# Performance work log

Hardware: AMD Instinct MI355X
Metric: run time of the kernel (lower is better)

Reference implementation:

```python
import jax, jax.numpy as jnp
import numpy as np

N_IN = 512
N_OUT = 256
K = 3
GRID_SIZE = N_OUT - K + 1  # 254
X_LO, X_HI = -1.0, 1.0
BATCH = 1024
LN_EPS = 1e-5


def make_grid():
    # grid_values: (n_in, grid_size + 2k + 1), identical rows as in the torch module
    step = (X_HI - X_LO) / GRID_SIZE
    g = jnp.linspace(X_LO - step * K, X_HI + step * K, GRID_SIZE + 2 * K + 1, dtype=jnp.float32)
    return jnp.broadcast_to(g, (N_IN, g.shape[0]))


def setup_inputs() -> dict:
    key = jax.random.key(0)
    k1, k2, k3 = jax.random.split(key, 3)
    x = jax.random.normal(k1, (BATCH, N_IN), dtype=jnp.float32)
    # kaiming-uniform-like scale for the linear weights
    weights = jax.random.normal(k2, (N_OUT, N_IN), dtype=jnp.float32) * (1.0 / np.sqrt(N_IN))
    spline_weights = jax.random.normal(k3, (N_OUT, N_IN, GRID_SIZE + K), dtype=jnp.float32) * (
        1.0 / np.sqrt(N_IN * (GRID_SIZE + K))
    )
    prelu_a = jnp.full((1,), 0.25, dtype=jnp.float32)  # PReLU default init
    return {"x": x, "weights": weights, "spline_weights": spline_weights, "prelu_a": prelu_a}


def reference(x, weights, spline_weights, prelu_a):
    g = make_grid()  # (n_in, P) with P = GRID_SIZE + 2K + 1
    # base branch: tanh(x) @ W^T
    b_out = jnp.tanh(x) @ weights.T  # (B, n_out)

    # Cox-de Boor recursion for B-spline bases
    xe = x[:, :, None]  # (B, n_in, 1)
    bases = ((xe >= g[:, :-1]) & (xe < g[:, 1:])).astype(x.dtype)  # (B, n_in, P-1)
    for k in range(1, K + 1):
        left = g[:, : -(k + 1)]
        right = g[:, k:-1]
        delta = jnp.where(right == left, jnp.ones_like(right), right - left)
        bases = (xe - left) / delta * bases[:, :, :-1] + (
            (g[:, k + 1 :] - xe) / (g[:, k + 1 :] - g[:, 1:-k])
        ) * bases[:, :, 1:]
    # bases: (B, n_in, GRID_SIZE + K)

    # flattened linear == einsum over (n_in, grid) axes
    spline_out = jnp.einsum("big,oig->bo", bases, spline_weights)  # (B, n_out)

    y = b_out + spline_out
    # LayerNorm without affine params
    mu = jnp.mean(y, axis=-1, keepdims=True)
    var = jnp.var(y, axis=-1, keepdims=True)
    yn = (y - mu) / jnp.sqrt(var + LN_EPS)
    # PReLU (single shared slope)
    return jnp.where(yn >= 0, yn, prelu_a[0] * yn)
```

## Files before the change

### kernel.cpp

```cpp
#include <hip/hip_runtime.h>
#include <hip/hip_fp16.h>
#include <math.h>

#define N_IN   512
#define N_OUT  256
#define NCOEF  257
#define BATCH  1024
#define LN_EPS 1e-5f
#define G0F (-1.0f - 3.0f * (2.0f / 254.0f))

#define ROWQ 20
#define NQ   129
#define SLABW (NQ * ROWQ)

#define SLOT(q_, oo_) ((q_) * ROWQ + (((((oo_) >> 2) ^ ((q_) & 3))) << 2) + ((oo_) & 3))

static __device__ __forceinline__ unsigned pk_bf16x2(float a, float b) {
    unsigned ua = ((__float_as_uint(a) + 0x8000u) >> 16) & 0xffffu;
    unsigned ub = (__float_as_uint(b) + 0x8000u) & 0xffff0000u;
    return ua | ub;
}

static __device__ __forceinline__ float dot2bf(unsigned w, unsigned s, float c) {
    float d;
    asm("v_dot2_f32_bf16 %0, %1, %2, %3" : "=v"(d) : "v"(w), "v"(s), "v"(c));
    return d;
}

static __device__ __forceinline__ uint4 spline_pack(float xv) {
    const float e2 = __expf(2.f * xv);
    const float tx = 1.f - 2.f / (e2 + 1.f);
    const float u  = (xv - G0F) * 127.f;
    const bool has = (u >= 0.f) && (u < 260.f);
    const float uf = has ? u : 0.f;
    int m = (int)uf;
    if (m > 259) m = 259;
    const float tt = uf - (float)m;
    const float t2 = tt * tt, t3 = t2 * tt;
    const float omt = 1.f - tt;
    float a0 = omt * omt * omt * (1.f / 6.f);
    float a1 = (3.f * t3 - 6.f * t2 + 4.f) * (1.f / 6.f);
    float a2 = (-3.f * t3 + 3.f * t2 + 3.f * tt + 1.f) * (1.f / 6.f);
    float a3 = t3 * (1.f / 6.f);
    if (!has) { a0 = a1 = a2 = a3 = 0.f; }
    const int pb  = m - 3;
    const int pbc = pb < 0 ? 0 : (pb > 253 ? 253 : pb);
    const int d   = pbc - pb;
    if (d >= 1)  { a0 = a1; a1 = a2; a2 = a3; a3 = 0.f; }
    if (d >= 2)  { a0 = a1; a1 = a2; a2 = a3; a3 = 0.f; }
    if (d >= 3)  { a0 = a1; a1 = a2; a2 = a3; a3 = 0.f; }
    if (d <= -1) { a3 = a2; a2 = a1; a1 = a0; a0 = 0.f; }
    if (d <= -2) { a3 = a2; a2 = a1; a1 = a0; a0 = 0.f; }
    if (d <= -3) { a3 = a2; a2 = a1; a1 = a0; a0 = 0.f; }
    uint4 r;
    if (pbc & 1) {
        r.x = pk_bf16x2(0.f, a0);
        r.y = pk_bf16x2(a1, a2);
        r.z = pk_bf16x2(a3, 0.f);
    } else {
        r.x = pk_bf16x2(a0, a1);
        r.y = pk_bf16x2(a2, a3);
        r.z = 0u;
    }
    r.w = (unsigned)(pbc & ~1) |
          ((unsigned)__half_as_ushort(__float2half(tx)) << 16);
    return r;
}

__global__ __launch_bounds__(1024, 4) void kan_main(
    const float* __restrict__ x, const float* __restrict__ W,
    const float* __restrict__ sw, float* __restrict__ part)
{
    const int bid = blockIdx.x;
    const int oc = bid & 15;
    const int ig = bid >> 4;
    const int o0 = oc * 16, i0 = ig * 32;
    const int t = threadIdx.x;

    __shared__ __align__(16) unsigned slab[2][2][SLABW];
    __shared__ __align__(16) uint4 wpk[2][1024];
    __shared__ float Wl[2][2][16];

    const int wv = t >> 6, l = t & 63;
    const int bl = (l >> 2) & 15, og = l & 3;
    const int soo = t & 15;
    const int sgc = t >> 4;
    const int wsub = t >> 4;

    const float* swrow = sw + ((size_t)(o0 + soo) * N_IN + i0) * NCOEF;
    const float* xp    = x + (size_t)t * N_IN + i0;
    const float* wgp   = W + (size_t)(o0 + (t & 15)) * N_IN + i0 + wsub;

    float4 pf0, pf1;
    float sT0 = 0.f, sT1 = 0.f, Wc = 0.f;
    float2 xn;

#define GLOAD(p) do {                                             \
        const float* _r0 = swrow + (size_t)(2 * (p)) * NCOEF;     \
        const float* _r1 = _r0 + NCOEF;                           \
        pf0 = *(const float4*)&_r0[sgc * 4];                      \
        pf1 = *(const float4*)&_r1[sgc * 4];                      \
        if (sgc == 63) { sT0 = _r0[256]; sT1 = _r1[256]; }        \
    } while (0)

#define STAGE(wb) do {                                            \
        const int _q = 2 * sgc;                                   \
        unsigned* _s0 = &slab[wb][0][0];                          \
        unsigned* _s1 = &slab[wb][1][0];                          \
        _s0[SLOT(_q,     soo)] = pk_bf16x2(pf0.x, pf0.y);         \
        _s0[SLOT(_q + 1, soo)] = pk_bf16x2(pf0.z, pf0.w);         \
        _s1[SLOT(_q,     soo)] = pk_bf16x2(pf1.x, pf1.y);         \
        _s1[SLOT(_q + 1, soo)] = pk_bf16x2(pf1.z, pf1.w);         \
        if (sgc == 63) {                                          \
            _s0[SLOT(128, soo)] = pk_bf16x2(sT0, 0.f);            \
            _s1[SLOT(128, soo)] = pk_bf16x2(sT1, 0.f);            \
        }                                                         \
    } while (0)

    GLOAD(0);
    xn = *(const float2*)&xp[0];
    if (t < 32) Wc = wgp[0];
    STAGE(0);
    if (t < 32) Wl[0][wsub][t & 15] = Wc;
    wpk[0][t] = spline_pack(xn.x);
    wpk[1][t] = spline_pack(xn.y);
    GLOAD(1);
    xn = *(const float2*)&xp[2];
    if (t < 32) Wc = wgp[2];

    float4 acc[4];
#pragma unroll
    for (int bp = 0; bp < 4; ++bp) acc[bp] = make_float4(0.f, 0.f, 0.f, 0.f);

    __syncthreads();

    int buf = 0;
    for (int n = 0; n < 16; ++n) {
#pragma unroll
        for (int sub = 0; sub < 2; ++sub) {
            const float4 Wv = *(const float4*)&Wl[buf][sub][og << 2];
            const unsigned* sl = &slab[buf][sub][0];
#pragma unroll
            for (int bp = 0; bp < 4; ++bp) {
                const uint4 u = wpk[sub][wv * 64 + (bp << 4) + bl];
                const float tx =
                    __half2float(__ushort_as_half((unsigned short)(u.w >> 16)));
                float4 a = acc[bp];
                a.x = fmaf(tx, Wv.x, a.x);
                a.y = fmaf(tx, Wv.y, a.y);
                a.z = fmaf(tx, Wv.z, a.z);
                a.w = fmaf(tx, Wv.w, a.w);
                if (u.x | u.y | u.z) {
                    const int q0 = (int)(u.w & 0xffffu) >> 1;
#pragma unroll
                    for (int j = 0; j < 3; ++j) {
                        const int q = q0 + j;
                        const int ad = q * ROWQ + ((og ^ (q & 3)) << 2);
                        const uint4 s4 = *(const uint4*)&sl[ad];
                        const unsigned wj = (j == 0) ? u.x : (j == 1) ? u.y : u.z;
                        a.x = dot2bf(wj, s4.x, a.x);
                        a.y = dot2bf(wj, s4.y, a.y);
                        a.z = dot2bf(wj, s4.z, a.z);
                        a.w = dot2bf(wj, s4.w, a.w);
                    }
                }
                acc[bp] = a;
            }
        }

        if (n + 1 < 16) {
            STAGE(buf ^ 1);
            if (t < 32) Wl[buf ^ 1][wsub][t & 15] = Wc;
            wpk[0][t] = spline_pack(xn.x);
            wpk[1][t] = spline_pack(xn.y);
            if (n + 2 < 16) {
                GLOAD(n + 2);
                xn = *(const float2*)&xp[2 * (n + 2)];
                if (t < 32) Wc = wgp[2 * (n + 2)];
            }
        }
        __syncthreads();
        buf ^= 1;
    }

    float* dst = part + ((size_t)ig * BATCH) * N_OUT + o0 + (og << 2);
#pragma unroll
    for (int bp = 0; bp < 4; ++bp) {
        const int lb = wv * 64 + (bp << 4) + bl;
        *reinterpret_cast<float4*>(&dst[(size_t)lb * N_OUT]) = acc[bp];
    }
#undef GLOAD
#undef STAGE
}

__global__ __launch_bounds__(256) void kan_ln(
    const float* __restrict__ part, const float* __restrict__ prelu_a,
    float* __restrict__ out)
{
    const int b = blockIdx.x;
    const int t = threadIdx.x;

    float sv = 0.f;
#pragma unroll
    for (int k = 0; k < 16; ++k)
        sv += part[((size_t)k * BATCH + b) * N_OUT + t];

    float v1 = sv, v2 = sv * sv;
#pragma unroll
    for (int d = 1; d < 64; d <<= 1) {
        v1 += __shfl_xor(v1, d);
        v2 += __shfl_xor(v2, d);
    }
    __shared__ float r1[4], r2[4];
    if ((t & 63) == 0) { r1[t >> 6] = v1; r2[t >> 6] = v2; }
    __syncthreads();
    const float tot1 = r1[0] + r1[1] + r1[2] + r1[3];
    const float tot2 = r2[0] + r2[1] + r2[2] + r2[3];

    const float mu  = tot1 * (1.f / N_OUT);
    const float var = tot2 * (1.f / N_OUT) - mu * mu;
    const float inv = rsqrtf(var + LN_EPS);
    const float yn  = (sv - mu) * inv;
    const float a   = prelu_a[0];
    out[(size_t)b * N_OUT + t] = (yn >= 0.f) ? yn : a * yn;
}

extern "C" void kernel_launch(void* const* d_in, const int* in_sizes, int n_in,
                              void* d_out, int out_size, void* d_ws, size_t ws_size,
                              hipStream_t stream)
{
    const float* x  = (const float*)d_in[0];
    const float* W  = (const float*)d_in[1];
    const float* sw = (const float*)d_in[2];
    const float* pa = (const float*)d_in[3];
    float* out  = (float*)d_out;
    float* part = (float*)d_ws;

    kan_main<<<dim3(256), 1024, 0, stream>>>(x, W, sw, part);
    kan_ln  <<<dim3(1024), 256, 0, stream>>>(part, pa, out);
}
```

Measured before the change: 90.05 us.

## Split batch across blocks and give each thread one row with all sixteen outputs

The main kernel now launches twice as many 512-thread blocks, each covering half the batch, so each thread owns one batch row and accumulates all 16 outputs in registers. Each thread computes its spline basis itself instead of staging packed bases in shared memory. The base-branch weights are read straight from global memory rather than through shared memory. The staging barrier now sits only at the end of each step and the next slab is written before compute. In exchange, every block reloads the spline-weight slab, doubling that global traffic. Register pressure also rises and all lanes of a wave read different slab rows, which may add LDS bank conflicts.

```diff
diff --git a/kernel.cpp b/kernel.cpp
--- a/kernel.cpp
+++ b/kernel.cpp
@@ -67,128 +67,121 @@
     return r;
 }
 
-__global__ __launch_bounds__(1024, 4) void kan_main(
+__global__ __launch_bounds__(512, 4) void kan_main(
     const float* __restrict__ x, const float* __restrict__ W,
     const float* __restrict__ sw, float* __restrict__ part)
 {
     const int bid = blockIdx.x;
-    const int oc = bid & 15;
-    const int ig = bid >> 4;
-    const int o0 = oc * 16, i0 = ig * 32;
+    const int bc = bid & 1;
+    const int oc = (bid >> 1) & 15;
+    const int ig = bid >> 5;
+    const int o0 = oc * 16, i0 = ig * 32, b0 = bc * 512;
     const int t = threadIdx.x;
 
     __shared__ __align__(16) unsigned slab[2][2][SLABW];
-    __shared__ __align__(16) uint4 wpk[2][1024];
-    __shared__ float Wl[2][2][16];
-
-    const int wv = t >> 6, l = t & 63;
-    const int bl = (l >> 2) & 15, og = l & 3;
+
     const int soo = t & 15;
     const int sgc = t >> 4;
-    const int wsub = t >> 4;
 
     const float* swrow = sw + ((size_t)(o0 + soo) * N_IN + i0) * NCOEF;
-    const float* xp    = x + (size_t)t * N_IN + i0;
-    const float* wgp   = W + (size_t)(o0 + (t & 15)) * N_IN + i0 + wsub;
-
-    float4 pf0, pf1;
-    float sT0 = 0.f, sT1 = 0.f, Wc = 0.f;
-    float2 xn;
+    const float* xp    = x + (size_t)(b0 + t) * N_IN + i0;
+
+    float4 A0, B0, A1, B1;
+    float t0 = 0.f, t1 = 0.f;
+    float2 xc, xn, x2;
 
 #define GLOAD(p) do {                                             \
         const float* _r0 = swrow + (size_t)(2 * (p)) * NCOEF;     \
         const float* _r1 = _r0 + NCOEF;                           \
-        pf0 = *(const float4*)&_r0[sgc * 4];                      \
-        pf1 = *(const float4*)&_r1[sgc * 4];                      \
-        if (sgc == 63) { sT0 = _r0[256]; sT1 = _r1[256]; }        \
+        A0 = *(const float4*)&_r0[sgc * 4];                       \
+        B0 = *(const float4*)&_r0[sgc * 4 + 128];                 \
+        A1 = *(const float4*)&_r1[sgc * 4];                       \
+        B1 = *(const float4*)&_r1[sgc * 4 + 128];                 \
+        if (sgc == 31) { t0 = _r0[256]; t1 = _r1[256]; }          \
     } while (0)
 
 #define STAGE(wb) do {                                            \
-        const int _q = 2 * sgc;                                   \
         unsigned* _s0 = &slab[wb][0][0];                          \
         unsigned* _s1 = &slab[wb][1][0];                          \
-        _s0[SLOT(_q,     soo)] = pk_bf16x2(pf0.x, pf0.y);         \
-        _s0[SLOT(_q + 1, soo)] = pk_bf16x2(pf0.z, pf0.w);         \
-        _s1[SLOT(_q,     soo)] = pk_bf16x2(pf1.x, pf1.y);         \
-        _s1[SLOT(_q + 1, soo)] = pk_bf16x2(pf1.z, pf1.w);         \
-        if (sgc == 63) {                                          \
-            _s0[SLOT(128, soo)] = pk_bf16x2(sT0, 0.f);            \
-            _s1[SLOT(128, soo)] = pk_bf16x2(sT1, 0.f);            \
+        const int _qa = 2 * sgc;                                  \
+        _s0[SLOT(_qa,      soo)] = pk_bf16x2(A0.x, A0.y);         \
+        _s0[SLOT(_qa + 1,  soo)] = pk_bf16x2(A0.z, A0.w);         \
+        _s0[SLOT(_qa + 64, soo)] = pk_bf16x2(B0.x, B0.y);         \
+        _s0[SLOT(_qa + 65, soo)] = pk_bf16x2(B0.z, B0.w);         \
+        _s1[SLOT(_qa,      soo)] = pk_bf16x2(A1.x, A1.y);         \
+        _s1[SLOT(_qa + 1,  soo)] = pk_bf16x2(A1.z, A1.w);         \
+        _s1[SLOT(_qa + 64, soo)] = pk_bf16x2(B1.x, B1.y);         \
+        _s1[SLOT(_qa + 65, soo)] = pk_bf16x2(B1.z, B1.w);         \
+        if (sgc == 31) {                                          \
+            _s0[SLOT(128, soo)] = pk_bf16x2(t0, 0.f);             \
+            _s1[SLOT(128, soo)] = pk_bf16x2(t1, 0.f);             \
         }                                                         \
     } while (0)
 
+    float acc[16];
+#pragma unroll
+    for (int oo = 0; oo < 16; ++oo) acc[oo] = 0.f;
+
     GLOAD(0);
-    xn = *(const float2*)&xp[0];
-    if (t < 32) Wc = wgp[0];
+    xc = *(const float2*)&xp[0];
     STAGE(0);
-    if (t < 32) Wl[0][wsub][t & 15] = Wc;
-    wpk[0][t] = spline_pack(xn.x);
-    wpk[1][t] = spline_pack(xn.y);
     GLOAD(1);
     xn = *(const float2*)&xp[2];
-    if (t < 32) Wc = wgp[2];
-
-    float4 acc[4];
-#pragma unroll
-    for (int bp = 0; bp < 4; ++bp) acc[bp] = make_float4(0.f, 0.f, 0.f, 0.f);
-
+    x2 = xn;
     __syncthreads();
 
     int buf = 0;
     for (int n = 0; n < 16; ++n) {
+        if (n + 1 < 16) {
+            STAGE(buf ^ 1);
+            if (n + 2 < 16) {
+                GLOAD(n + 2);
+                x2 = *(const float2*)&xp[2 * (n + 2)];
+            }
+        }
+
 #pragma unroll
         for (int sub = 0; sub < 2; ++sub) {
-            const float4 Wv = *(const float4*)&Wl[buf][sub][og << 2];
-            const unsigned* sl = &slab[buf][sub][0];
-#pragma unroll
-            for (int bp = 0; bp < 4; ++bp) {
-                const uint4 u = wpk[sub][wv * 64 + (bp << 4) + bl];
-                const float tx =
-                    __half2float(__ushort_as_half((unsigned short)(u.w >> 16)));
-                float4 a = acc[bp];
-                a.x = fmaf(tx, Wv.x, a.x);
-                a.y = fmaf(tx, Wv.y, a.y);
-                a.z = fmaf(tx, Wv.z, a.z);
-                a.w = fmaf(tx, Wv.w, a.w);
-                if (u.x | u.y | u.z) {
-                    const int q0 = (int)(u.w & 0xffffu) >> 1;
-#pragma unroll
-                    for (int j = 0; j < 3; ++j) {
-                        const int q = q0 + j;
-                        const int ad = q * ROWQ + ((og ^ (q & 3)) << 2);
-                        const uint4 s4 = *(const uint4*)&sl[ad];
-                        const unsigned wj = (j == 0) ? u.x : (j == 1) ? u.y : u.z;
-                        a.x = dot2bf(wj, s4.x, a.x);
-                        a.y = dot2bf(wj, s4.y, a.y);
-                        a.z = dot2bf(wj, s4.z, a.z);
-                        a.w = dot2bf(wj, s4.w, a.w);
+            const int i = i0 + 2 * n + sub;
+            const uint4 u = spline_pack(sub == 0 ? xc.x : xc.y);
+            const float tx =
+                __half2float(__ushort_as_half((unsigned short)(u.w >> 16)));
+            const float* Wrow = W + (size_t)o0 * N_IN + i;
+#pragma unroll
+            for (int oo = 0; oo < 16; ++oo)
+                acc[oo] = fmaf(tx, Wrow[(size_t)oo * N_IN], acc[oo]);
+            if (u.x | u.y | u.z) {
+                const int q0 = (int)(u.w & 0xffffu) >> 1;
+                const unsigned* sl = &slab[buf][sub][0];
+#pragma unroll
+                for (int j = 0; j < 3; ++j) {
+                    const int q = q0 + j;
+                    const unsigned wj = (j == 0) ? u.x : (j == 1) ? u.y : u.z;
+                    const unsigned* row = sl + q * ROWQ;
+                    const int m = q & 3;
+#pragma unroll
+                    for (int lq = 0; lq < 4; ++lq) {
+                        const uint4 s4 = *(const uint4*)&row[(lq ^ m) << 2];
+                        acc[lq * 4 + 0] = dot2bf(wj, s4.x, acc[lq * 4 + 0]);
+                        acc[lq * 4 + 1] = dot2bf(wj, s4.y, acc[lq * 4 + 1]);
+                        acc[lq * 4 + 2] = dot2bf(wj, s4.z, acc[lq * 4 + 2]);
+                        acc[lq * 4 + 3] = dot2bf(wj, s4.w, acc[lq * 4 + 3]);
                     }
                 }
-                acc[bp] = a;
             }
         }
 
-        if (n + 1 < 16) {
-            STAGE(buf ^ 1);
-            if (t < 32) Wl[buf ^ 1][wsub][t & 15] = Wc;
-            wpk[0][t] = spline_pack(xn.x);
-            wpk[1][t] = spline_pack(xn.y);
-            if (n + 2 < 16) {
-                GLOAD(n + 2);
-                xn = *(const float2*)&xp[2 * (n + 2)];
-                if (t < 32) Wc = wgp[2 * (n + 2)];
-            }
-        }
         __syncthreads();
         buf ^= 1;
+        xc = xn;
+        xn = x2;
     }
 
-    float* dst = part + ((size_t)ig * BATCH) * N_OUT + o0 + (og << 2);
-#pragma unroll
-    for (int bp = 0; bp < 4; ++bp) {
-        const int lb = wv * 64 + (bp << 4) + bl;
-        *reinterpret_cast<float4*>(&dst[(size_t)lb * N_OUT]) = acc[bp];
-    }
+    float* dst = part + ((size_t)ig * BATCH + b0 + t) * N_OUT + o0;
+#pragma unroll
+    for (int v = 0; v < 4; ++v)
+        *reinterpret_cast<float4*>(&dst[v * 4]) =
+            make_float4(acc[v * 4], acc[v * 4 + 1], acc[v * 4 + 2], acc[v * 4 + 3]);
 #undef GLOAD
 #undef STAGE
 }
@@ -236,6 +229,6 @@
     float* out  = (float*)d_out;
     float* part = (float*)d_ws;
 
-    kan_main<<<dim3(256), 1024, 0, stream>>>(x, W, sw, part);
+    kan_main<<<dim3(512), 512, 0, stream>>>(x, W, sw, part);
     kan_ln  <<<dim3(1024), 256, 0, stream>>>(part, pa, out);
 }
```

New measurement: 98.46 us. 9.3% more time.
